# Optimization experiments

Measured on AMD Instinct MI355X. Metric: run time of the kernel, lower is better.

Reference implementation:

```python
import jax, jax.numpy as jnp
import numpy as np

B, SQ, HIDDEN = 2, 2048, 2048
HEADS, GROUPS, KVC = 16, 4, 128
HPG = HEADS // GROUPS          # heads per group
LAYER_INDEX = 1
SCALE = KVC ** -0.5            # attention_softmax_scale_power = 0.5


def setup_inputs() -> dict:
    key = jax.random.key(0)
    k1, k2, k3, k4 = jax.random.split(key, 4)
    return {
        "x": jax.random.normal(k1, (B, SQ, HIDDEN), jnp.float32),
        "w_q": jax.random.normal(k2, (HIDDEN, HEADS * KVC), jnp.float32) * 0.02,
        "w_kv": jax.random.normal(k3, (HIDDEN, 2 * GROUPS * KVC), jnp.float32) * 0.02,
        "w_dense": jax.random.normal(k4, (HEADS * KVC, HIDDEN), jnp.float32) * 0.02,
    }


def reference(x, w_q, w_kv, w_dense):
    b, sq, _ = x.shape
    sk = sq
    # QKV projections
    q = jnp.einsum("bsh,he->bse", x, w_q).reshape(b, sq, GROUPS, HPG, KVC)
    kv = jnp.einsum("bsh,he->bse", x, w_kv)
    k, v = jnp.split(kv, 2, axis=-1)
    k = k.reshape(b, sk, GROUPS, KVC)
    v = v.reshape(b, sk, GROUPS, KVC)
    # scaled QK^T with the per-layer scale trick: alpha = scale/L in input
    # dtype, then cast to fp32 and multiply by L (as in _attn_fused)
    scores = jnp.einsum("bqgpd,bkgd->bgqpk", q, k) * (SCALE / LAYER_INDEX)
    scores = scores.astype(jnp.float32) * LAYER_INDEX
    # causal mask: mask = ~triu(ones, diagonal=1) -> keep where q_idx >= k_idx
    causal = (jnp.arange(sq)[:, None] >= jnp.arange(sk)[None, :])
    scores = jnp.where(causal[None, None, :, None, :], scores, -jnp.inf)
    probs = jax.nn.softmax(scores, axis=-1).astype(x.dtype)
    # dropout p = 0.0 -> no-op
    ctx = jnp.einsum("bgqpk,bkgd->bqgpd", probs, v).reshape(b, sq, HEADS * KVC)
    return jnp.einsum("bse,eh->bsh", ctx, w_dense)
```

## Files before the change

### kernel.cpp

```cpp
#include <hip/hip_runtime.h>
#include <hip/hip_bf16.h>


typedef __attribute__((ext_vector_type(4))) float f32x4;
typedef __attribute__((ext_vector_type(8))) short bf16x8;
typedef __attribute__((ext_vector_type(4))) short bf16x4;

__device__ __forceinline__ unsigned short f2bf(float f) {
    unsigned u = __builtin_bit_cast(unsigned, f);
    unsigned r = u + 0x7fffu + ((u >> 16) & 1u);
    return (unsigned short)(r >> 16);
}

__device__ __forceinline__ unsigned cvtpk_bf16(float lo, float hi) {
    unsigned r;
    asm("v_cvt_pk_bf16_f32 %0, %1, %2" : "=v"(r) : "v"(lo), "v"(hi));
    return r;
}

__device__ __forceinline__ void gl_lds16(const void* g, void* l) {
    __builtin_amdgcn_global_load_lds(
        (const __attribute__((address_space(1))) unsigned int*)g,
        (__attribute__((address_space(3))) unsigned int*)l, 16, 0, 0);
}

__global__ __launch_bounds__(256)
void xcvt_kernel(const float* __restrict__ in, unsigned short* __restrict__ out)
{
    size_t i = ((size_t)blockIdx.x * 256 + threadIdx.x) * 8;
    float4 a = *reinterpret_cast<const float4*>(&in[i]);
    float4 b = *reinterpret_cast<const float4*>(&in[i + 4]);
    bf16x8 o = { (short)f2bf(a.x), (short)f2bf(a.y),
                 (short)f2bf(a.z), (short)f2bf(a.w),
                 (short)f2bf(b.x), (short)f2bf(b.y),
                 (short)f2bf(b.z), (short)f2bf(b.w) };
    *reinterpret_cast<bf16x8*>(&out[i]) = o;
}

__global__ __launch_bounds__(256)
void wtrans_kernel(const float* __restrict__ in, unsigned short* __restrict__ out,
                   int K, int N)
{
    __shared__ unsigned short T[64][72];
    const int n0 = blockIdx.x * 64, k0 = blockIdx.y * 64;
    const int tid = threadIdx.x;
#pragma unroll
    for (int i = 0; i < 4; ++i) {
        int f = tid + i * 256;
        int r = f >> 4;
        int c4 = (f & 15) * 4;
        float4 v = *reinterpret_cast<const float4*>(&in[(size_t)(k0 + r) * N + n0 + c4]);
        bf16x4 pk = { (short)f2bf(v.x), (short)f2bf(v.y),
                      (short)f2bf(v.z), (short)f2bf(v.w) };
        *reinterpret_cast<bf16x4*>(&T[r][c4]) = pk;
    }
    __syncthreads();
#pragma unroll
    for (int i = 0; i < 2; ++i) {
        int f = tid + i * 256;
        int nn = f >> 3;
        int s8 = (f & 7) * 8;
        bf16x8 o;
#pragma unroll
        for (int j = 0; j < 8; ++j) o[j] = T[s8 + j][nn];
        *reinterpret_cast<bf16x8*>(&out[(size_t)(n0 + nn) * K + k0 + s8]) = o;
    }
}

__global__ __launch_bounds__(256)
void gemm_qkv_kernel(const unsigned short* __restrict__ A,
                     const unsigned short* __restrict__ BT,
                     void* __restrict__ C0v, void* __restrict__ C1v,
                     int M, int N, int K)
{
    __shared__ __align__(16) unsigned short Alds[3][128 * 32];
    __shared__ __align__(16) unsigned short Blds[3][128 * 32];

    const int tid = threadIdx.x;
    const int lane = tid & 63;
    const int wid = tid >> 6;
    const int wr = wid >> 1, wc = wid & 1;
    const int m0 = blockIdx.y * 128;
    const int n0 = blockIdx.x * 128;
    const int l16 = lane & 15, lg = lane >> 4;

    f32x4 acc[4][4];
#pragma unroll
    for (int m = 0; m < 4; ++m)
#pragma unroll
        for (int n = 0; n < 4; ++n) acc[m][n] = (f32x4){0.f, 0.f, 0.f, 0.f};

    int srow[2], skb[2];
#pragma unroll
    for (int i = 0; i < 2; ++i) {
        int L = i * 4096 + tid * 16;
        int R = L >> 7, c = L & 127;
        int cp = c ^ ((R & 7) << 4);
        srow[i] = 2 * R + (cp >> 6);
        skb[i]  = cp & 63;
    }

    auto stage = [&](int kt, int bi) {
#pragma unroll
        for (int i = 0; i < 2; ++i) {
            int L = i * 4096 + tid * 16;
            gl_lds16((const char*)A + ((size_t)(m0 + srow[i]) * K + kt) * 2 + skb[i],
                     (char*)(&Alds[bi][0]) + L);
            gl_lds16((const char*)BT + ((size_t)(n0 + srow[i]) * K + kt) * 2 + skb[i],
                     (char*)(&Blds[bi][0]) + L);
        }
    };

    const int NK = K / 32;
    stage(0, 0);
    stage(32, 1);

    for (int t = 0; t < NK; ++t) {
        const int bi = t % 3;
        if (t + 2 < NK) {
            stage((t + 2) * 32, (t + 2) % 3);
            asm volatile("s_waitcnt vmcnt(8)" ::: "memory");
        } else if (t + 1 < NK) {
            asm volatile("s_waitcnt vmcnt(4)" ::: "memory");
        } else {
            asm volatile("s_waitcnt vmcnt(0)" ::: "memory");
        }
        __builtin_amdgcn_s_barrier();

        const char* Ab = (const char*)(&Alds[bi][0]);
        const char* Bb = (const char*)(&Blds[bi][0]);

        bf16x8 af[4], bf[4];
#pragma unroll
        for (int m = 0; m < 4; ++m) {
            int row = wr * 64 + m * 16 + l16;
            int byte = (row >> 1) * 128 +
                       ((((row & 1) << 6) + lg * 16) ^ (((row >> 1) & 7) << 4));
            af[m] = *reinterpret_cast<const bf16x8*>(Ab + byte);
        }
#pragma unroll
        for (int n = 0; n < 4; ++n) {
            int row = wc * 64 + n * 16 + l16;
            int byte = (row >> 1) * 128 +
                       ((((row & 1) << 6) + lg * 16) ^ (((row >> 1) & 7) << 4));
            bf[n] = *reinterpret_cast<const bf16x8*>(Bb + byte);
        }
#pragma unroll
        for (int m = 0; m < 4; ++m)
#pragma unroll
            for (int n = 0; n < 4; ++n)
                acc[m][n] = __builtin_amdgcn_mfma_f32_16x16x32_bf16(
                    af[m], bf[n], acc[m][n], 0, 0, 0);

        __builtin_amdgcn_s_barrier();
    }

#pragma unroll
    for (int m = 0; m < 4; ++m) {
#pragma unroll
        for (int n = 0; n < 4; ++n) {
#pragma unroll
            for (int r = 0; r < 4; ++r) {
                int row = m0 + wr * 64 + m * 16 + lg * 4 + r;
                int col = n0 + wc * 64 + n * 16 + l16;
                float val = acc[m][n][r];
                if (n0 < 2048)
                    ((unsigned short*)C0v)[(size_t)row * 2048 + col] =
                        f2bf(val * 0.12751879523209208f);
                else
                    ((unsigned short*)C1v)[(size_t)row * 1024 + (col - 2048)] = f2bf(val);
            }
        }
    }
}

__global__ __launch_bounds__(256)
void gemm_dense_kernel(const unsigned short* __restrict__ A,
                       const unsigned short* __restrict__ BT,
                       float* __restrict__ C, int M, int N, int K)
{
    __shared__ __align__(16) unsigned short Alds[2][128 * 64];
    __shared__ __align__(16) unsigned short Blds[2][128 * 64];

    const int tid = threadIdx.x;
    const int lane = tid & 63;
    const int wid = tid >> 6;
    const int wr = wid >> 1, wc = wid & 1;
    const int m0 = blockIdx.y * 128;
    const int n0 = blockIdx.x * 128;
    const int l16 = lane & 15, lg = lane >> 4;

    f32x4 acc[4][4];
#pragma unroll
    for (int m = 0; m < 4; ++m)
#pragma unroll
        for (int n = 0; n < 4; ++n) acc[m][n] = (f32x4){0.f, 0.f, 0.f, 0.f};

    auto stage = [&](int kt, int bi) {
#pragma unroll
        for (int i = 0; i < 4; ++i) {
            int row = i * 32 + (tid >> 3);
            int cb = ((tid & 7) * 16) ^ ((row & 7) << 4);
            gl_lds16((const char*)A + ((size_t)(m0 + row) * K + kt) * 2 + cb,
                     (char*)(&Alds[bi][0]) + i * 4096 + wid * 1024);
            gl_lds16((const char*)BT + ((size_t)(n0 + row) * K + kt) * 2 + cb,
                     (char*)(&Blds[bi][0]) + i * 4096 + wid * 1024);
        }
    };

    const int NK = K / 64;
    stage(0, 0);
    int cur = 0;

    for (int kti = 0; kti < NK; ++kti) {
        if (kti + 1 < NK) {
            stage((kti + 1) * 64, cur ^ 1);
            asm volatile("s_waitcnt vmcnt(8)" ::: "memory");
        } else {
            asm volatile("s_waitcnt vmcnt(0)" ::: "memory");
        }
        __builtin_amdgcn_s_barrier();

        const char* Ab = (const char*)(&Alds[cur][0]);
        const char* Bb = (const char*)(&Blds[cur][0]);

        bf16x8 af[2][4], bf[2][4];
#pragma unroll
        for (int kd = 0; kd < 2; ++kd) {
#pragma unroll
            for (int m = 0; m < 4; ++m) {
                int row = wr * 64 + m * 16 + l16;
                af[kd][m] = *reinterpret_cast<const bf16x8*>(
                    Ab + row * 128 + ((kd * 64 + lg * 16) ^ ((row & 7) << 4)));
            }
#pragma unroll
            for (int n = 0; n < 4; ++n) {
                int row = wc * 64 + n * 16 + l16;
                bf[kd][n] = *reinterpret_cast<const bf16x8*>(
                    Bb + row * 128 + ((kd * 64 + lg * 16) ^ ((row & 7) << 4)));
            }
        }
#pragma unroll
        for (int kd = 0; kd < 2; ++kd)
#pragma unroll
            for (int m = 0; m < 4; ++m)
#pragma unroll
                for (int n = 0; n < 4; ++n)
                    acc[m][n] = __builtin_amdgcn_mfma_f32_16x16x32_bf16(
                        af[kd][m], bf[kd][n], acc[m][n], 0, 0, 0);

        __builtin_amdgcn_s_barrier();
        cur ^= 1;
    }

#pragma unroll
    for (int m = 0; m < 4; ++m) {
#pragma unroll
        for (int n = 0; n < 4; ++n) {
#pragma unroll
            for (int r = 0; r < 4; ++r) {
                int row = m0 + wr * 64 + m * 16 + lg * 4 + r;
                int col = n0 + wc * 64 + n * 16 + l16;
                C[(size_t)row * N + col] = acc[m][n][r];
            }
        }
    }
}

__global__ __launch_bounds__(256)
void vtrans_kernel(const unsigned short* __restrict__ kv,
                   unsigned short* __restrict__ vt)
{
    __shared__ unsigned short T[64][140];
    const int bg = blockIdx.y;
    const int b = bg >> 2, g = bg & 3;
    const int s0 = blockIdx.x * 64;
    const int tid = threadIdx.x;

#pragma unroll
    for (int i = 0; i < 4; ++i) {
        int f = tid + i * 256;
        int sl = f >> 4;
        int d0 = (f & 15) * 8;
        bf16x8 v = *reinterpret_cast<const bf16x8*>(
            &kv[(size_t)(b * 2048 + s0 + sl) * 1024 + 512 + g * 128 + d0]);
        bf16x4 lo = { v[0], v[1], v[2], v[3] };
        bf16x4 hi = { v[4], v[5], v[6], v[7] };
        *reinterpret_cast<bf16x4*>(&T[sl][d0])     = lo;
        *reinterpret_cast<bf16x4*>(&T[sl][d0 + 4]) = hi;
    }
    __syncthreads();
#pragma unroll
    for (int i = 0; i < 4; ++i) {
        int f = tid + i * 256;
        int d = f >> 3;
        int s8 = (f & 7) * 8;
        bf16x8 o;
#pragma unroll
        for (int j = 0; j < 8; ++j) o[j] = T[s8 + j][d];
        *reinterpret_cast<bf16x8*>(
            &vt[(size_t)(bg * 128 + d) * 2048 + s0 + s8]) = o;
    }
}

__global__ __launch_bounds__(256)
void attn_kernel(const unsigned short* __restrict__ Q,
                 const unsigned short* __restrict__ KV,
                 const unsigned short* __restrict__ VT,
                 unsigned short* __restrict__ CTX)
{
    constexpr int SQ = 2048;
    __shared__ __align__(16) unsigned short Klds[2][64 * 128];
    __shared__ __align__(16) unsigned short Vlds[2][128 * 64];
    __shared__ __align__(16) unsigned short Pl[4][16][64];

    const int tid = threadIdx.x;
    const int lane = tid & 63;
    const int w = tid >> 6;
    const int l16 = lane & 15, lg = lane >> 4;

    const int bid = blockIdx.x;
    const int gb = bid & 7;
    const int g = gb & 3, b = gb >> 2;
    const int pi = bid >> 3;
    const int hh = g * 4 + w;

    const size_t qbase = (size_t)b * SQ * 2048;
    const char* KVb = (const char*)KV + (size_t)b * SQ * 2048;
    const char* VTb = (const char*)VT;

    const int pswz = (l16 & 7) << 3;

    auto stage = [&](int t, int bi) {
        const int k0 = t * 64;
#pragma unroll
        for (int i = 0; i < 4; ++i) {
            int row = w * 16 + i * 4 + (lane >> 4);
            int scol = ((lane & 15) * 16) ^ ((row & 7) << 4);
            gl_lds16(KVb + (size_t)(k0 + row) * 2048 + g * 256 + scol,
                     (char*)(&Klds[bi][0]) + w * 4096 + i * 1024);
        }
#pragma unroll
        for (int i = 0; i < 4; ++i) {
            int row = w * 32 + i * 8 + (lane >> 3);
            int scol = ((lane & 7) * 16) ^ ((row & 7) << 4);
            gl_lds16(VTb + ((size_t)(gb * 128 + row) * 2048 + k0) * 2 + scol,
                     (char*)(&Vlds[bi][0]) + w * 4096 + i * 1024);
        }
    };

#pragma unroll 1
    for (int seg = 0; seg < 2; ++seg) {
        const int qt = seg ? pi : (127 - pi);
        const int ntiles = qt / 4 + 1;

        bf16x8 qfrag[4];
#pragma unroll
        for (int kd = 0; kd < 4; ++kd)
            qfrag[kd] = *reinterpret_cast<const bf16x8*>(
                &Q[qbase + (size_t)(qt * 16 + l16) * 2048 + hh * 128 + kd * 32 + lg * 8]);

        float lsum = 0.f;
        f32x4 acc[8];
#pragma unroll
        for (int nd = 0; nd < 8; ++nd) acc[nd] = (f32x4){0.f,0.f,0.f,0.f};

        stage(0, 0);

        for (int t = 0; t < ntiles; ++t) {
            const int bi = t & 1;
            const int k0 = t * 64;
            if (t + 1 < ntiles) {
                stage(t + 1, bi ^ 1);
                asm volatile("s_waitcnt vmcnt(8)" ::: "memory");
            } else {
                asm volatile("s_waitcnt vmcnt(0)" ::: "memory");
            }
            __builtin_amdgcn_s_barrier();

            const char* Kb = (const char*)(&Klds[bi][0]);
            const char* Vb = (const char*)(&Vlds[bi][0]);

            f32x4 st[4];
#pragma unroll
            for (int nf = 0; nf < 4; ++nf) st[nf] = (f32x4){0.f,0.f,0.f,0.f};
            __builtin_amdgcn_s_setprio(1);
#pragma unroll
            for (int nf = 0; nf < 4; ++nf) {
                int row = nf * 16 + l16;
#pragma unroll
                for (int kd = 0; kd < 4; ++kd) {
                    bf16x8 kf = *reinterpret_cast<const bf16x8*>(
                        Kb + row * 256 + ((kd * 64 + lg * 16) ^ ((row & 7) << 4)));
                    st[nf] = __builtin_amdgcn_mfma_f32_16x16x32_bf16(
                        kf, qfrag[kd], st[nf], 0, 0, 0);
                }
            }
            __builtin_amdgcn_s_setprio(0);

            const bool diag = (t == ntiles - 1);
            {
                float lacc = 0.f;
                const int q = qt * 16 + l16;
#pragma unroll
                for (int nf = 0; nf < 4; ++nf) {
                    float cs0 = st[nf][0];
                    float cs1 = st[nf][1];
                    float cs2 = st[nf][2];
                    float cs3 = st[nf][3];
                    if (diag) {
                        const int keyb = k0 + nf * 16 + lg * 4;
                        if (keyb + 0 > q) cs0 = -INFINITY;
                        if (keyb + 1 > q) cs1 = -INFINITY;
                        if (keyb + 2 > q) cs2 = -INFINITY;
                        if (keyb + 3 > q) cs3 = -INFINITY;
                    }
                    float p0 = exp2f(cs0), p1 = exp2f(cs1);
                    float p2 = exp2f(cs2), p3 = exp2f(cs3);
                    lacc += (p0 + p1) + (p2 + p3);
                    uint2 pk = { cvtpk_bf16(p0, p1), cvtpk_bf16(p2, p3) };
                    *reinterpret_cast<uint2*>(
                        &Pl[w][l16][(nf * 16 + lg * 4) ^ pswz]) = pk;
                }
                lacc += __shfl_xor(lacc, 16, 64);
                lacc += __shfl_xor(lacc, 32, 64);
                lsum += lacc;
            }

            __builtin_amdgcn_s_setprio(1);
#pragma unroll
            for (int kc = 0; kc < 2; ++kc) {
                bf16x8 pf = *reinterpret_cast<const bf16x8*>(
                    &Pl[w][l16][(kc * 32 + lg * 8) ^ pswz]);
#pragma unroll
                for (int nd = 0; nd < 8; ++nd) {
                    int row = nd * 16 + l16;
                    bf16x8 vf = *reinterpret_cast<const bf16x8*>(
                        Vb + row * 128 + ((kc * 64 + lg * 16) ^ ((row & 7) << 4)));
                    acc[nd] = __builtin_amdgcn_mfma_f32_16x16x32_bf16(
                        vf, pf, acc[nd], 0, 0, 0);
                }
            }
            __builtin_amdgcn_s_setprio(0);
            __builtin_amdgcn_s_barrier();
        }

        {
            float inv = 1.0f / lsum;
            const int q = qt * 16 + l16;
#pragma unroll
            for (int nd = 0; nd < 8; ++nd) {
                bf16x4 o = { (short)f2bf(acc[nd][0] * inv),
                             (short)f2bf(acc[nd][1] * inv),
                             (short)f2bf(acc[nd][2] * inv),
                             (short)f2bf(acc[nd][3] * inv) };
                *reinterpret_cast<bf16x4*>(
                    &CTX[qbase + (size_t)q * 2048 + hh * 128 + nd * 16 + lg * 4]) = o;
            }
        }
    }
}

extern "C" void kernel_launch(void* const* d_in, const int* in_sizes, int n_in,
                              void* d_out, int out_size, void* d_ws, size_t ws_size,
                              hipStream_t stream)
{
    const float* x       = (const float*)d_in[0];
    const float* w_q     = (const float*)d_in[1];
    const float* w_kv    = (const float*)d_in[2];
    const float* w_dense = (const float*)d_in[3];

    const int M = 4096;

    char* ws = (char*)d_ws;
    unsigned short* kv_buf  = (unsigned short*)(ws);
    unsigned short* ctx_buf = (unsigned short*)(ws + (8u << 20));
    unsigned short* wqT     = (unsigned short*)(ws + (24u << 20));
    unsigned short* wkvT    = (unsigned short*)(ws + (32u << 20));
    unsigned short* wdT     = wqT;
    unsigned short* xbf    = (unsigned short*)d_out;
    unsigned short* q_buf  = (unsigned short*)d_out + (size_t)M * 2048;
    unsigned short* vt_buf = (unsigned short*)d_out;

    dim3 blk(256);
    xcvt_kernel<<<dim3(4096), blk, 0, stream>>>(x, xbf);
    wtrans_kernel<<<dim3(32, 32), blk, 0, stream>>>(w_q, wqT, 2048, 2048);
    wtrans_kernel<<<dim3(16, 32), blk, 0, stream>>>(w_kv, wkvT, 2048, 1024);
    gemm_qkv_kernel<<<dim3(24, 32), blk, 0, stream>>>(
        xbf, wqT, (void*)q_buf, (void*)kv_buf, M, 3072, 2048);
    wtrans_kernel<<<dim3(32, 32), blk, 0, stream>>>(w_dense, wdT, 2048, 2048);
    vtrans_kernel<<<dim3(32, 8), blk, 0, stream>>>(kv_buf, vt_buf);
    attn_kernel<<<dim3(512), blk, 0, stream>>>(q_buf, kv_buf, vt_buf, ctx_buf);
    gemm_dense_kernel<<<dim3(16, 32), blk, 0, stream>>>(
        ctx_buf, wdT, (float*)d_out, M, 2048, 2048);
}
```

Baseline: 190.5 us.

## Process paired causal query tiles together to share K/V tile loads

The attention kernel used to process its two query tiles (a long one and a short one from opposite ends of the causal range) one after the other, loading K/V twice. It now runs them in a single key loop that shares each staged K/V tile: both tiles get their MFMAs while the short tile still has keys, then only the long one continues. The intent is to cut global loads and barriers for the overlapping prefix and to interleave independent MFMA chains. In exchange it doubles the accumulator registers and the P buffer in LDS, which may lower occupancy. The block-to-pair mapping is also reordered.

```diff
diff --git a/kernel.cpp b/kernel.cpp
--- a/kernel.cpp
+++ b/kernel.cpp
@@ -312,7 +312,7 @@
     constexpr int SQ = 2048;
     __shared__ __align__(16) unsigned short Klds[2][64 * 128];
     __shared__ __align__(16) unsigned short Vlds[2][128 * 64];
-    __shared__ __align__(16) unsigned short Pl[4][16][64];
+    __shared__ __align__(16) unsigned short Pl[4][2][16][64];
 
     const int tid = threadIdx.x;
     const int lane = tid & 63;
@@ -322,7 +322,12 @@
     const int bid = blockIdx.x;
     const int gb = bid & 7;
     const int g = gb & 3, b = gb >> 2;
-    const int pi = bid >> 3;
+    const int idx = bid >> 3;
+    const int pi = (idx < 32) ? idx : 63 - (idx - 32);
+    const int qtA = 127 - pi;
+    const int qtB = pi;
+    const int ntA = qtA / 4 + 1;
+    const int ntB = qtB / 4 + 1;
     const int hh = g * 4 + w;
 
     const size_t qbase = (size_t)b * SQ * 2048;
@@ -349,41 +354,75 @@
         }
     };
 
-#pragma unroll 1
-    for (int seg = 0; seg < 2; ++seg) {
-        const int qt = seg ? pi : (127 - pi);
-        const int ntiles = qt / 4 + 1;
-
-        bf16x8 qfrag[4];
-#pragma unroll
-        for (int kd = 0; kd < 4; ++kd)
-            qfrag[kd] = *reinterpret_cast<const bf16x8*>(
-                &Q[qbase + (size_t)(qt * 16 + l16) * 2048 + hh * 128 + kd * 32 + lg * 8]);
-
-        float lsum = 0.f;
-        f32x4 acc[8];
-#pragma unroll
-        for (int nd = 0; nd < 8; ++nd) acc[nd] = (f32x4){0.f,0.f,0.f,0.f};
-
-        stage(0, 0);
-
-        for (int t = 0; t < ntiles; ++t) {
-            const int bi = t & 1;
-            const int k0 = t * 64;
-            if (t + 1 < ntiles) {
-                stage(t + 1, bi ^ 1);
-                asm volatile("s_waitcnt vmcnt(8)" ::: "memory");
-            } else {
-                asm volatile("s_waitcnt vmcnt(0)" ::: "memory");
-            }
-            __builtin_amdgcn_s_barrier();
-
-            const char* Kb = (const char*)(&Klds[bi][0]);
-            const char* Vb = (const char*)(&Vlds[bi][0]);
-
-            f32x4 st[4];
-#pragma unroll
-            for (int nf = 0; nf < 4; ++nf) st[nf] = (f32x4){0.f,0.f,0.f,0.f};
+    bf16x8 qfA[4], qfB[4];
+#pragma unroll
+    for (int kd = 0; kd < 4; ++kd) {
+        qfA[kd] = *reinterpret_cast<const bf16x8*>(
+            &Q[qbase + (size_t)(qtA * 16 + l16) * 2048 + hh * 128 + kd * 32 + lg * 8]);
+        qfB[kd] = *reinterpret_cast<const bf16x8*>(
+            &Q[qbase + (size_t)(qtB * 16 + l16) * 2048 + hh * 128 + kd * 32 + lg * 8]);
+    }
+
+    float lsumA = 0.f, lsumB = 0.f;
+    f32x4 accA[8], accB[8];
+#pragma unroll
+    for (int nd = 0; nd < 8; ++nd) {
+        accA[nd] = (f32x4){0.f,0.f,0.f,0.f};
+        accB[nd] = (f32x4){0.f,0.f,0.f,0.f};
+    }
+
+    auto softmax = [&](f32x4 (&st)[4], int qt, bool diag, int k0, int mslot,
+                       float& lsum) {
+        float lacc = 0.f;
+        const int q = qt * 16 + l16;
+#pragma unroll
+        for (int nf = 0; nf < 4; ++nf) {
+            float cs0 = st[nf][0];
+            float cs1 = st[nf][1];
+            float cs2 = st[nf][2];
+            float cs3 = st[nf][3];
+            if (diag) {
+                const int keyb = k0 + nf * 16 + lg * 4;
+                if (keyb + 0 > q) cs0 = -INFINITY;
+                if (keyb + 1 > q) cs1 = -INFINITY;
+                if (keyb + 2 > q) cs2 = -INFINITY;
+                if (keyb + 3 > q) cs3 = -INFINITY;
+            }
+            float p0 = exp2f(cs0), p1 = exp2f(cs1);
+            float p2 = exp2f(cs2), p3 = exp2f(cs3);
+            lacc += (p0 + p1) + (p2 + p3);
+            uint2 pk = { cvtpk_bf16(p0, p1), cvtpk_bf16(p2, p3) };
+            *reinterpret_cast<uint2*>(
+                &Pl[w][mslot][l16][(nf * 16 + lg * 4) ^ pswz]) = pk;
+        }
+        lacc += __shfl_xor(lacc, 16, 64);
+        lacc += __shfl_xor(lacc, 32, 64);
+        lsum += lacc;
+    };
+
+    stage(0, 0);
+
+    for (int t = 0; t < ntA; ++t) {
+        const int bi = t & 1;
+        const int k0 = t * 64;
+        if (t + 1 < ntA) {
+            stage(t + 1, bi ^ 1);
+            asm volatile("s_waitcnt vmcnt(8)" ::: "memory");
+        } else {
+            asm volatile("s_waitcnt vmcnt(0)" ::: "memory");
+        }
+        __builtin_amdgcn_s_barrier();
+
+        const char* Kb = (const char*)(&Klds[bi][0]);
+        const char* Vb = (const char*)(&Vlds[bi][0]);
+
+        if (t < ntB) {
+            f32x4 stA[4], stB[4];
+#pragma unroll
+            for (int nf = 0; nf < 4; ++nf) {
+                stA[nf] = (f32x4){0.f,0.f,0.f,0.f};
+                stB[nf] = (f32x4){0.f,0.f,0.f,0.f};
+            }
             __builtin_amdgcn_s_setprio(1);
 #pragma unroll
             for (int nf = 0; nf < 4; ++nf) {
@@ -392,71 +431,99 @@
                 for (int kd = 0; kd < 4; ++kd) {
                     bf16x8 kf = *reinterpret_cast<const bf16x8*>(
                         Kb + row * 256 + ((kd * 64 + lg * 16) ^ ((row & 7) << 4)));
-                    st[nf] = __builtin_amdgcn_mfma_f32_16x16x32_bf16(
-                        kf, qfrag[kd], st[nf], 0, 0, 0);
+                    stA[nf] = __builtin_amdgcn_mfma_f32_16x16x32_bf16(
+                        kf, qfA[kd], stA[nf], 0, 0, 0);
+                    stB[nf] = __builtin_amdgcn_mfma_f32_16x16x32_bf16(
+                        kf, qfB[kd], stB[nf], 0, 0, 0);
                 }
             }
             __builtin_amdgcn_s_setprio(0);
 
-            const bool diag = (t == ntiles - 1);
-            {
-                float lacc = 0.f;
-                const int q = qt * 16 + l16;
-#pragma unroll
-                for (int nf = 0; nf < 4; ++nf) {
-                    float cs0 = st[nf][0];
-                    float cs1 = st[nf][1];
-                    float cs2 = st[nf][2];
-                    float cs3 = st[nf][3];
-                    if (diag) {
-                        const int keyb = k0 + nf * 16 + lg * 4;
-                        if (keyb + 0 > q) cs0 = -INFINITY;
-                        if (keyb + 1 > q) cs1 = -INFINITY;
-                        if (keyb + 2 > q) cs2 = -INFINITY;
-                        if (keyb + 3 > q) cs3 = -INFINITY;
-                    }
-                    float p0 = exp2f(cs0), p1 = exp2f(cs1);
-                    float p2 = exp2f(cs2), p3 = exp2f(cs3);
-                    lacc += (p0 + p1) + (p2 + p3);
-                    uint2 pk = { cvtpk_bf16(p0, p1), cvtpk_bf16(p2, p3) };
-                    *reinterpret_cast<uint2*>(
-                        &Pl[w][l16][(nf * 16 + lg * 4) ^ pswz]) = pk;
-                }
-                lacc += __shfl_xor(lacc, 16, 64);
-                lacc += __shfl_xor(lacc, 32, 64);
-                lsum += lacc;
-            }
+            softmax(stA, qtA, t == ntA - 1, k0, 0, lsumA);
+            softmax(stB, qtB, t == ntB - 1, k0, 1, lsumB);
 
             __builtin_amdgcn_s_setprio(1);
 #pragma unroll
             for (int kc = 0; kc < 2; ++kc) {
-                bf16x8 pf = *reinterpret_cast<const bf16x8*>(
-                    &Pl[w][l16][(kc * 32 + lg * 8) ^ pswz]);
+                bf16x8 pfA = *reinterpret_cast<const bf16x8*>(
+                    &Pl[w][0][l16][(kc * 32 + lg * 8) ^ pswz]);
+                bf16x8 pfB = *reinterpret_cast<const bf16x8*>(
+                    &Pl[w][1][l16][(kc * 32 + lg * 8) ^ pswz]);
 #pragma unroll
                 for (int nd = 0; nd < 8; ++nd) {
                     int row = nd * 16 + l16;
                     bf16x8 vf = *reinterpret_cast<const bf16x8*>(
                         Vb + row * 128 + ((kc * 64 + lg * 16) ^ ((row & 7) << 4)));
-                    acc[nd] = __builtin_amdgcn_mfma_f32_16x16x32_bf16(
-                        vf, pf, acc[nd], 0, 0, 0);
+                    accA[nd] = __builtin_amdgcn_mfma_f32_16x16x32_bf16(
+                        vf, pfA, accA[nd], 0, 0, 0);
+                    accB[nd] = __builtin_amdgcn_mfma_f32_16x16x32_bf16(
+                        vf, pfB, accB[nd], 0, 0, 0);
                 }
             }
             __builtin_amdgcn_s_setprio(0);
-            __builtin_amdgcn_s_barrier();
-        }
-
-        {
-            float inv = 1.0f / lsum;
-            const int q = qt * 16 + l16;
-#pragma unroll
-            for (int nd = 0; nd < 8; ++nd) {
-                bf16x4 o = { (short)f2bf(acc[nd][0] * inv),
-                             (short)f2bf(acc[nd][1] * inv),
-                             (short)f2bf(acc[nd][2] * inv),
-                             (short)f2bf(acc[nd][3] * inv) };
-                *reinterpret_cast<bf16x4*>(
-                    &CTX[qbase + (size_t)q * 2048 + hh * 128 + nd * 16 + lg * 4]) = o;
-            }
+        } else {
+            f32x4 stA[4];
+#pragma unroll
+            for (int nf = 0; nf < 4; ++nf) stA[nf] = (f32x4){0.f,0.f,0.f,0.f};
+            __builtin_amdgcn_s_setprio(1);
+#pragma unroll
+            for (int nf = 0; nf < 4; ++nf) {
+                int row = nf * 16 + l16;
+#pragma unroll
+                for (int kd = 0; kd < 4; ++kd) {
+                    bf16x8 kf = *reinterpret_cast<const bf16x8*>(
+                        Kb + row * 256 + ((kd * 64 + lg * 16) ^ ((row & 7) << 4)));
+                    stA[nf] = __builtin_amdgcn_mfma_f32_16x16x32_bf16(
+                        kf, qfA[kd], stA[nf], 0, 0, 0);
+                }
+            }
+            __builtin_amdgcn_s_setprio(0);
+
+            softmax(stA, qtA, t == ntA - 1, k0, 0, lsumA);
+
+            __builtin_amdgcn_s_setprio(1);
+#pragma unroll
+            for (int kc = 0; kc < 2; ++kc) {
+                bf16x8 pfA = *reinterpret_cast<const bf16x8*>(
+                    &Pl[w][0][l16][(kc * 32 + lg * 8) ^ pswz]);
+#pragma unroll
+                for (int nd = 0; nd < 8; ++nd) {
+                    int row = nd * 16 + l16;
+                    bf16x8 vf = *reinterpret_cast<const bf16x8*>(
+                        Vb + row * 128 + ((kc * 64 + lg * 16) ^ ((row & 7) << 4)));
+                    accA[nd] = __builtin_amdgcn_mfma_f32_16x16x32_bf16(
+                        vf, pfA, accA[nd], 0, 0, 0);
+                }
+            }
+            __builtin_amdgcn_s_setprio(0);
+        }
+        __builtin_amdgcn_s_barrier();
+    }
+
+    {
+        float inv = 1.0f / lsumA;
+        const int q = qtA * 16 + l16;
+#pragma unroll
+        for (int nd = 0; nd < 8; ++nd) {
+            bf16x4 o = { (short)f2bf(accA[nd][0] * inv),
+                         (short)f2bf(accA[nd][1] * inv),
+                         (short)f2bf(accA[nd][2] * inv),
+                         (short)f2bf(accA[nd][3] * inv) };
+            *reinterpret_cast<bf16x4*>(
+                &CTX[qbase + (size_t)q * 2048 + hh * 128 + nd * 16 + lg * 4]) = o;
+        }
+    }
+    {
+        float inv = 1.0f / lsumB;
+        const int q = qtB * 16 + l16;
+#pragma unroll
+        for (int nd = 0; nd < 8; ++nd) {
+            bf16x4 o = { (short)f2bf(accB[nd][0] * inv),
+                         (short)f2bf(accB[nd][1] * inv),
+                         (short)f2bf(accB[nd][2] * inv),
+                         (short)f2bf(accB[nd][3] * inv) };
+            *reinterpret_cast<bf16x4*>(
+                &CTX[qbase + (size_t)q * 2048 + hh * 128 + nd * 16 + lg * 4]) = o;
         }
     }
 }
```

Measured after the change: 240.6 us. +26.3%, slower.

## Switch attention to 32x32 MFMA with waves split across two query tiles

Applied to the files above, without the earlier changes.

The attention kernel moves from 16x16x32 to 32x32x16 bf16 MFMA, packing two heads (16 rows each) into one 32-row MFMA operand. Each wave now takes a 16-row slice of one of two paired query tiles (long and short causal tiles). The block streams the longer tile's key range while waves on the shorter tile idle once they finish. This is meant to raise MFMA efficiency and halve K/V LDS reads per head pair. In exchange the block count, causal load balance and register pressure all change, and waves on the short tile sit idle through the later iterations.

```diff
diff --git a/kernel.cpp b/kernel.cpp
--- a/kernel.cpp
+++ b/kernel.cpp
@@ -3,6 +3,7 @@
 
 
 typedef __attribute__((ext_vector_type(4))) float f32x4;
+typedef __attribute__((ext_vector_type(16))) float f32x16;
 typedef __attribute__((ext_vector_type(8))) short bf16x8;
 typedef __attribute__((ext_vector_type(4))) short bf16x4;
 
@@ -312,24 +313,35 @@
     constexpr int SQ = 2048;
     __shared__ __align__(16) unsigned short Klds[2][64 * 128];
     __shared__ __align__(16) unsigned short Vlds[2][128 * 64];
-    __shared__ __align__(16) unsigned short Pl[4][16][64];
+    __shared__ __align__(16) unsigned short Pl[4][32][64];
 
     const int tid = threadIdx.x;
     const int lane = tid & 63;
     const int w = tid >> 6;
-    const int l16 = lane & 15, lg = lane >> 4;
+    const int c = lane & 31;
+    const int hi = lane >> 5;
 
     const int bid = blockIdx.x;
     const int gb = bid & 7;
     const int g = gb & 3, b = gb >> 2;
-    const int pi = bid >> 3;
-    const int hh = g * 4 + w;
+    const int rest = bid >> 3;
+    const int hp = rest & 1;
+    const int idx = rest >> 1;
+    const int pi = (idx < 16) ? idx : 31 - (idx - 16);
+    const int tw = w >> 1;
+    const int qt = tw ? pi : (63 - pi);
+    const int ntA = (63 - pi) / 2 + 1;
+    const int ntB = pi / 2 + 1;
+    const int nt = tw ? ntB : ntA;
+    const int sub = (w & 1) * 16;
+    const int head = g * 4 + hp * 2 + (c >> 4);
+    const int qrow = qt * 32 + sub + (c & 15);
 
     const size_t qbase = (size_t)b * SQ * 2048;
     const char* KVb = (const char*)KV + (size_t)b * SQ * 2048;
     const char* VTb = (const char*)VT;
 
-    const int pswz = (l16 & 7) << 3;
+    const int pswz = (c & 7) << 4;
 
     auto stage = [&](int t, int bi) {
         const int k0 = t * 64;
@@ -349,113 +361,112 @@
         }
     };
 
-#pragma unroll 1
-    for (int seg = 0; seg < 2; ++seg) {
-        const int qt = seg ? pi : (127 - pi);
-        const int ntiles = qt / 4 + 1;
-
-        bf16x8 qfrag[4];
-#pragma unroll
-        for (int kd = 0; kd < 4; ++kd)
-            qfrag[kd] = *reinterpret_cast<const bf16x8*>(
-                &Q[qbase + (size_t)(qt * 16 + l16) * 2048 + hh * 128 + kd * 32 + lg * 8]);
-
-        float lsum = 0.f;
-        f32x4 acc[8];
-#pragma unroll
-        for (int nd = 0; nd < 8; ++nd) acc[nd] = (f32x4){0.f,0.f,0.f,0.f};
-
-        stage(0, 0);
-
-        for (int t = 0; t < ntiles; ++t) {
-            const int bi = t & 1;
-            const int k0 = t * 64;
-            if (t + 1 < ntiles) {
-                stage(t + 1, bi ^ 1);
-                asm volatile("s_waitcnt vmcnt(8)" ::: "memory");
-            } else {
-                asm volatile("s_waitcnt vmcnt(0)" ::: "memory");
-            }
-            __builtin_amdgcn_s_barrier();
-
+    bf16x8 qf[8];
+#pragma unroll
+    for (int kd = 0; kd < 8; ++kd)
+        qf[kd] = *reinterpret_cast<const bf16x8*>(
+            &Q[qbase + (size_t)qrow * 2048 + head * 128 + kd * 16 + hi * 8]);
+
+    float lsum = 0.f;
+    f32x16 acc[4];
+#pragma unroll
+    for (int dg = 0; dg < 4; ++dg)
+#pragma unroll
+        for (int r = 0; r < 16; ++r) acc[dg][r] = 0.f;
+
+    stage(0, 0);
+
+    for (int t = 0; t < ntA; ++t) {
+        const int bi = t & 1;
+        const int k0 = t * 64;
+        if (t + 1 < ntA) {
+            stage(t + 1, bi ^ 1);
+            asm volatile("s_waitcnt vmcnt(8)" ::: "memory");
+        } else {
+            asm volatile("s_waitcnt vmcnt(0)" ::: "memory");
+        }
+        __builtin_amdgcn_s_barrier();
+
+        if (t < nt) {
             const char* Kb = (const char*)(&Klds[bi][0]);
             const char* Vb = (const char*)(&Vlds[bi][0]);
-
-            f32x4 st[4];
-#pragma unroll
-            for (int nf = 0; nf < 4; ++nf) st[nf] = (f32x4){0.f,0.f,0.f,0.f};
+            const bool diag = (t == nt - 1);
+
+            f32x16 st0, st1;
+#pragma unroll
+            for (int r = 0; r < 16; ++r) { st0[r] = 0.f; st1[r] = 0.f; }
             __builtin_amdgcn_s_setprio(1);
 #pragma unroll
-            for (int nf = 0; nf < 4; ++nf) {
-                int row = nf * 16 + l16;
-#pragma unroll
-                for (int kd = 0; kd < 4; ++kd) {
-                    bf16x8 kf = *reinterpret_cast<const bf16x8*>(
-                        Kb + row * 256 + ((kd * 64 + lg * 16) ^ ((row & 7) << 4)));
-                    st[nf] = __builtin_amdgcn_mfma_f32_16x16x32_bf16(
-                        kf, qfrag[kd], st[nf], 0, 0, 0);
-                }
+            for (int kd = 0; kd < 8; ++kd) {
+                int krow0 = c;
+                int krow1 = 32 + c;
+                bf16x8 kf0 = *reinterpret_cast<const bf16x8*>(
+                    Kb + krow0 * 256 + ((kd * 32 + hi * 16) ^ ((krow0 & 7) << 4)));
+                bf16x8 kf1 = *reinterpret_cast<const bf16x8*>(
+                    Kb + krow1 * 256 + ((kd * 32 + hi * 16) ^ ((krow1 & 7) << 4)));
+                st0 = __builtin_amdgcn_mfma_f32_32x32x16_bf16(kf0, qf[kd], st0, 0, 0, 0);
+                st1 = __builtin_amdgcn_mfma_f32_32x32x16_bf16(kf1, qf[kd], st1, 0, 0, 0);
             }
             __builtin_amdgcn_s_setprio(0);
 
-            const bool diag = (t == ntiles - 1);
             {
                 float lacc = 0.f;
-                const int q = qt * 16 + l16;
-#pragma unroll
-                for (int nf = 0; nf < 4; ++nf) {
-                    float cs0 = st[nf][0];
-                    float cs1 = st[nf][1];
-                    float cs2 = st[nf][2];
-                    float cs3 = st[nf][3];
-                    if (diag) {
-                        const int keyb = k0 + nf * 16 + lg * 4;
-                        if (keyb + 0 > q) cs0 = -INFINITY;
-                        if (keyb + 1 > q) cs1 = -INFINITY;
-                        if (keyb + 2 > q) cs2 = -INFINITY;
-                        if (keyb + 3 > q) cs3 = -INFINITY;
+#pragma unroll
+                for (int kf = 0; kf < 2; ++kf) {
+#pragma unroll
+                    for (int rq = 0; rq < 4; ++rq) {
+                        float p[4];
+#pragma unroll
+                        for (int j = 0; j < 4; ++j) {
+                            int key = k0 + kf * 32 + j + 8 * rq + 4 * hi;
+                            float cs = kf ? st1[rq * 4 + j] : st0[rq * 4 + j];
+                            if (diag && key > qrow) cs = -INFINITY;
+                            p[j] = exp2f(cs);
+                            lacc += p[j];
+                        }
+                        uint2 pk = { cvtpk_bf16(p[0], p[1]), cvtpk_bf16(p[2], p[3]) };
+                        int kbyte = (kf * 64 + rq * 16 + hi * 8) ^ pswz;
+                        *reinterpret_cast<uint2*>(
+                            (char*)(&Pl[w][0][0]) + c * 128 + kbyte) = pk;
                     }
-                    float p0 = exp2f(cs0), p1 = exp2f(cs1);
-                    float p2 = exp2f(cs2), p3 = exp2f(cs3);
-                    lacc += (p0 + p1) + (p2 + p3);
-                    uint2 pk = { cvtpk_bf16(p0, p1), cvtpk_bf16(p2, p3) };
-                    *reinterpret_cast<uint2*>(
-                        &Pl[w][l16][(nf * 16 + lg * 4) ^ pswz]) = pk;
                 }
-                lacc += __shfl_xor(lacc, 16, 64);
                 lacc += __shfl_xor(lacc, 32, 64);
                 lsum += lacc;
             }
 
             __builtin_amdgcn_s_setprio(1);
 #pragma unroll
-            for (int kc = 0; kc < 2; ++kc) {
+            for (int ks = 0; ks < 4; ++ks) {
                 bf16x8 pf = *reinterpret_cast<const bf16x8*>(
-                    &Pl[w][l16][(kc * 32 + lg * 8) ^ pswz]);
-#pragma unroll
-                for (int nd = 0; nd < 8; ++nd) {
-                    int row = nd * 16 + l16;
+                    (const char*)(&Pl[w][0][0]) + c * 128 +
+                    ((ks * 32 + hi * 16) ^ pswz));
+#pragma unroll
+                for (int dg = 0; dg < 4; ++dg) {
+                    int drow = dg * 32 + c;
                     bf16x8 vf = *reinterpret_cast<const bf16x8*>(
-                        Vb + row * 128 + ((kc * 64 + lg * 16) ^ ((row & 7) << 4)));
-                    acc[nd] = __builtin_amdgcn_mfma_f32_16x16x32_bf16(
-                        vf, pf, acc[nd], 0, 0, 0);
+                        Vb + drow * 128 + ((ks * 32 + hi * 16) ^ ((drow & 7) << 4)));
+                    acc[dg] = __builtin_amdgcn_mfma_f32_32x32x16_bf16(
+                        vf, pf, acc[dg], 0, 0, 0);
                 }
             }
             __builtin_amdgcn_s_setprio(0);
-            __builtin_amdgcn_s_barrier();
-        }
-
-        {
-            float inv = 1.0f / lsum;
-            const int q = qt * 16 + l16;
-#pragma unroll
-            for (int nd = 0; nd < 8; ++nd) {
-                bf16x4 o = { (short)f2bf(acc[nd][0] * inv),
-                             (short)f2bf(acc[nd][1] * inv),
-                             (short)f2bf(acc[nd][2] * inv),
-                             (short)f2bf(acc[nd][3] * inv) };
+        }
+        __builtin_amdgcn_s_barrier();
+    }
+
+    {
+        float inv = 1.0f / lsum;
+#pragma unroll
+        for (int dg = 0; dg < 4; ++dg) {
+#pragma unroll
+            for (int rq = 0; rq < 4; ++rq) {
+                int d0 = dg * 32 + rq * 8 + hi * 4;
+                bf16x4 o = { (short)f2bf(acc[dg][rq * 4 + 0] * inv),
+                             (short)f2bf(acc[dg][rq * 4 + 1] * inv),
+                             (short)f2bf(acc[dg][rq * 4 + 2] * inv),
+                             (short)f2bf(acc[dg][rq * 4 + 3] * inv) };
                 *reinterpret_cast<bf16x4*>(
-                    &CTX[qbase + (size_t)q * 2048 + hh * 128 + nd * 16 + lg * 4]) = o;
+                    &CTX[qbase + (size_t)qrow * 2048 + head * 128 + d0]) = o;
             }
         }
     }
```

After: 220.2 us. 15.6% more time.
